# Optimization experiments

Measured on AMD Instinct MI355X. Metric: run time of the kernel, lower is better.

The kernel has to match this reference:

```python
import jax, jax.numpy as jnp
import numpy as np

EPS = 1e-06


def setup_inputs() -> dict:
    key = jax.random.key(0)
    k1, k2 = jax.random.split(key)
    x = jax.random.normal(k1, (256, 4096), dtype=jnp.float32)
    # learned parameter, init matches torch.randn(...) * 0.1
    shapelets = jax.random.normal(k2, (8, 16, 128), dtype=jnp.float32) * 0.1
    return {"x": x, "shapelets": shapelets}


def reference(x, shapelets):
    B, T = x.shape
    C, Kc, L = shapelets.shape
    nwin = T - L + 1  # stride-1 unfold

    # sliding windows: [B, nwin, L] (same materialization as torch unfold)
    idx = jnp.arange(nwin)[:, None] + jnp.arange(L)[None, :]
    x_win = x[:, idx]

    # z-normalize each window (population std, unbiased=False)
    mu_x = jnp.mean(x_win, axis=2, keepdims=True)
    var_x = jnp.mean((x_win - mu_x) ** 2, axis=2, keepdims=True)
    std_x = jnp.sqrt(var_x) + EPS
    x_norm = (x_win - mu_x) / std_x

    # z-normalize shapelets per class/shapelet
    mu_s = jnp.mean(shapelets, axis=2, keepdims=True)
    var_s = jnp.mean((shapelets - mu_s) ** 2, axis=2, keepdims=True)
    std_s = jnp.sqrt(var_s) + EPS
    s_norm = (shapelets - mu_s) / std_s

    # normalized cross-correlation: [B, nwin, C, Kc]
    corr = jnp.einsum('btl,ckl->btck', x_norm, s_norm) / L

    # max over window positions, concat classes -> [B, C*Kc]
    max_vals = jnp.max(corr, axis=1)  # [B, C, Kc]
    return max_vals.reshape(B, C * Kc)
```

## Files before the change

kernel.cpp:

```cpp
#include <hip/hip_runtime.h>
#include <hip/hip_bf16.h>

typedef __attribute__((ext_vector_type(8))) short short8;
typedef __attribute__((ext_vector_type(4))) float float4v;

#define T_LEN 4096
#define L_LEN 128
#define NWIN  3969
#define CK    128

__device__ __forceinline__ unsigned short f2bf(float f) {
    unsigned u = __float_as_uint(f);
    u += 0x7fffu + ((u >> 16) & 1u);
    return (unsigned short)(u >> 16);
}

__global__ void prep_sh(const float* __restrict__ sh,
                        unsigned short* __restrict__ wsB) {
    const int ck = blockIdx.x;
    const int l  = threadIdx.x;
    __shared__ float rs[2], rq[2];
    const int lane = l & 63, wv = l >> 6;

    float v = sh[ck * L_LEN + l];
    float s = v, q = v * v;
    #pragma unroll
    for (int off = 32; off >= 1; off >>= 1) {
        s += __shfl_xor(s, off);
        q += __shfl_xor(q, off);
    }
    if (lane == 0) { rs[wv] = s; rq[wv] = q; }
    __syncthreads();
    float sm = rs[0] + rs[1], sq = rq[0] + rq[1];
    float mu  = sm * (1.f / L_LEN);
    float var = fmaxf(sq * (1.f / L_LEN) - mu * mu, 0.f);
    float inv = 1.f / (sqrtf(var) + 1e-6f);
    unsigned short b = f2bf((v - mu) * inv);
    const int nt = ck >> 4, n = ck & 15;
    const int kt = l >> 5, qd = (l >> 3) & 3, jj = l & 7;
    wsB[((((nt * 4 + kt) * 64) + qd * 16 + n) << 3) + jj] = b;
}

__global__ __launch_bounds__(512, 2)
void conv_row(const float* __restrict__ x,
              const unsigned short* __restrict__ wsB,
              float* __restrict__ out) {
    __shared__ alignas(16) unsigned short xb[8][T_LEN];
    __shared__ float sty[T_LEN];
    __shared__ float PSs[513], PQs[513];
    __shared__ float grpS[8], grpQ[8];
    __shared__ float wmax[8][CK];

    const int tid  = threadIdx.x;
    const int lane = tid & 63;
    const int wv   = tid >> 6;
    const int row  = blockIdx.x;
    const float4* xr4 = (const float4*)(x + row * T_LEN);

    short8 Bf[8][4];
    {
        const short8* Bp = (const short8*)wsB;
        #pragma unroll
        for (int nt = 0; nt < 8; ++nt)
            #pragma unroll
            for (int kt = 0; kt < 4; ++kt)
                Bf[nt][kt] = Bp[(nt * 4 + kt) * 64 + lane];
    }

    float v[16];
    {
        float4 a0 = xr4[2 * tid];
        float4 a1 = xr4[2 * tid + 1];
        float4 a2 = make_float4(0.f, 0.f, 0.f, 0.f), a3 = a2;
        if (tid < 511) { a2 = xr4[2 * tid + 2]; a3 = xr4[2 * tid + 3]; }
        v[0]=a0.x; v[1]=a0.y; v[2]=a0.z;  v[3]=a0.w;
        v[4]=a1.x; v[5]=a1.y; v[6]=a1.z;  v[7]=a1.w;
        v[8]=a2.x; v[9]=a2.y; v[10]=a2.z; v[11]=a2.w;
        v[12]=a3.x; v[13]=a3.y; v[14]=a3.z; v[15]=a3.w;
    }
    unsigned short bb[16];
    #pragma unroll
    for (int i = 0; i < 16; ++i) bb[i] = f2bf(v[i]);
    #pragma unroll
    for (int c = 0; c < 8; ++c) {
        short8 w8;
        #pragma unroll
        for (int j = 0; j < 8; ++j) w8[j] = (short)bb[c + j];
        *(short8*)&xb[c][8 * tid] = w8;
    }

    float s = 0.f, q = 0.f;
    #pragma unroll
    for (int i = 0; i < 8; ++i) { s += v[i]; q += v[i] * v[i]; }
    float is = s, iq = q;
    #pragma unroll
    for (int off = 1; off < 64; off <<= 1) {
        float ts = __shfl_up(is, off);
        float tq = __shfl_up(iq, off);
        if (lane >= off) { is += ts; iq += tq; }
    }
    if (lane == 63) { grpS[wv] = is; grpQ[wv] = iq; }
    __syncthreads();
    float os = 0.f, oq = 0.f;
    #pragma unroll
    for (int w = 0; w < 7; ++w) if (w < wv) { os += grpS[w]; oq += grpQ[w]; }
    PSs[tid] = os + is - s;
    PQs[tid] = oq + iq - q;
    if (tid == 511) { PSs[512] = os + is; PQs[512] = oq + iq; }
    __syncthreads();

    if (tid < 497) {
        float S = PSs[tid + 16] - PSs[tid];
        float Q = PQs[tid + 16] - PQs[tid];
        float4 b0 = make_float4(0.f, 0.f, 0.f, 0.f), b1 = b0;
        if (tid <= 495) { b0 = xr4[2 * tid + 32]; b1 = xr4[2 * tid + 33]; }
        float xn[8] = {b0.x, b0.y, b0.z, b0.w, b1.x, b1.y, b1.z, b1.w};
        #pragma unroll
        for (int e = 0; e < 8; ++e) {
            int w = 8 * tid + e;
            if (w < NWIN) {
                float mu  = S * (1.f / L_LEN);
                float var = fmaxf(Q * (1.f / L_LEN) - mu * mu, 0.f);
                float sd  = sqrtf(var) + 1e-6f;
                sty[w] = 1.f / (sd * (float)L_LEN);
                S += xn[e] - v[e];
                Q += xn[e] * xn[e] - v[e] * v[e];
            }
        }
    }
    __syncthreads();

    const int abase = (lane & 15) + (lane >> 4);
    const int q4    = (lane >> 4) * 4;
    float vmax[8];
    #pragma unroll
    for (int nt = 0; nt < 8; ++nt) vmax[nt] = -1e30f;

    #pragma unroll 1
    for (int ii = 0; ii < 32; ++ii) {
        const int ci = (ii + 4 * wv) & 31;
        const int T0 = (ci < 31) ? ci * 128 : (NWIN - 128);
        const int e0 = T0 + wv;
        const int c  = e0 & 7;
        const int b8 = e0 >> 3;

        float sr[4];
        #pragma unroll
        for (int r = 0; r < 4; ++r) sr[r] = sty[e0 + 8 * (q4 + r)];
        short8 af[4];
        #pragma unroll
        for (int kt = 0; kt < 4; ++kt)
            af[kt] = *(const short8*)&xb[c][8 * (b8 + abase + 4 * kt)];

        float4v acc[8];
        #pragma unroll
        for (int nt = 0; nt < 8; ++nt) acc[nt] = float4v{0.f, 0.f, 0.f, 0.f};

        #pragma unroll
        for (int kt = 0; kt < 4; ++kt)
            #pragma unroll
            for (int nt = 0; nt < 8; ++nt)
                acc[nt] = __builtin_amdgcn_mfma_f32_16x16x32_bf16(
                    af[kt], Bf[nt][kt], acc[nt], 0, 0, 0);

        #pragma unroll
        for (int nt = 0; nt < 8; ++nt) {
            float m01 = fmaxf(acc[nt][0] * sr[0], acc[nt][1] * sr[1]);
            float m23 = fmaxf(acc[nt][2] * sr[2], acc[nt][3] * sr[3]);
            vmax[nt] = fmaxf(vmax[nt], fmaxf(m01, m23));
        }
    }

    #pragma unroll
    for (int nt = 0; nt < 8; ++nt) {
        float vx = vmax[nt];
        vx = fmaxf(vx, __shfl_xor(vx, 16));
        vx = fmaxf(vx, __shfl_xor(vx, 32));
        if (lane < 16) wmax[wv][nt * 16 + lane] = vx;
    }
    __syncthreads();
    if (tid < CK) {
        float m = wmax[0][tid];
        #pragma unroll
        for (int w = 1; w < 8; ++w) m = fmaxf(m, wmax[w][tid]);
        out[row * CK + tid] = m;
    }
}

extern "C" void kernel_launch(void* const* d_in, const int* in_sizes, int n_in,
                              void* d_out, int out_size, void* d_ws, size_t ws_size,
                              hipStream_t stream) {
    (void)in_sizes; (void)n_in; (void)out_size; (void)ws_size;
    const float* x  = (const float*)d_in[0];
    const float* sh = (const float*)d_in[1];
    unsigned short* wsB = (unsigned short*)d_ws;
    float* out = (float*)d_out;

    prep_sh<<<128, 128, 0, stream>>>(sh, wsB);
    conv_row<<<256, 512, 0, stream>>>(x, wsB, out);
}
```

Measured before the change: 82.21 us.

## Split shapelet columns across two wave halves with 1024-thread blocks

Doubles the block to 1024 threads and splits the 128 output columns between two groups of 8 waves. Each wave now holds half the B fragments and issues half the MFMAs per window tile. The first 512 threads still do the staging and stats, and the final max reduction is regrouped by column half. This is meant to raise wave-level parallelism per row, which matters because only 256 blocks cover the GPU. It costs idle threads during staging and tighter register limits from the 1024,4 launch bounds.

```diff
diff --git a/kernel.cpp b/kernel.cpp
--- a/kernel.cpp
+++ b/kernel.cpp
@@ -41,7 +41,7 @@
     wsB[((((nt * 4 + kt) * 64) + qd * 16 + n) << 3) + jj] = b;
 }
 
-__global__ __launch_bounds__(512, 2)
+__global__ __launch_bounds__(1024, 4)
 void conv_row(const float* __restrict__ x,
               const unsigned short* __restrict__ wsB,
               float* __restrict__ out) {
@@ -49,26 +49,29 @@
     __shared__ float sty[T_LEN];
     __shared__ float PSs[513], PQs[513];
     __shared__ float grpS[8], grpQ[8];
-    __shared__ float wmax[8][CK];
+    __shared__ float wmax[16][64];
 
     const int tid  = threadIdx.x;
     const int lane = tid & 63;
     const int wv   = tid >> 6;
     const int row  = blockIdx.x;
     const float4* xr4 = (const float4*)(x + row * T_LEN);
-
-    short8 Bf[8][4];
+    const bool stg = (tid < 512);
+
+    const int mg = wv & 7, nh = wv >> 3;
+    short8 Bf[4][4];
     {
         const short8* Bp = (const short8*)wsB;
         #pragma unroll
-        for (int nt = 0; nt < 8; ++nt)
+        for (int nt4 = 0; nt4 < 4; ++nt4)
             #pragma unroll
             for (int kt = 0; kt < 4; ++kt)
-                Bf[nt][kt] = Bp[(nt * 4 + kt) * 64 + lane];
+                Bf[nt4][kt] = Bp[((nh * 4 + nt4) * 4 + kt) * 64 + lane];
     }
 
     float v[16];
-    {
+    float s = 0.f, q = 0.f;
+    if (stg) {
         float4 a0 = xr4[2 * tid];
         float4 a1 = xr4[2 * tid + 1];
         float4 a2 = make_float4(0.f, 0.f, 0.f, 0.f), a3 = a2;
@@ -77,36 +80,43 @@
         v[4]=a1.x; v[5]=a1.y; v[6]=a1.z;  v[7]=a1.w;
         v[8]=a2.x; v[9]=a2.y; v[10]=a2.z; v[11]=a2.w;
         v[12]=a3.x; v[13]=a3.y; v[14]=a3.z; v[15]=a3.w;
-    }
-    unsigned short bb[16];
-    #pragma unroll
-    for (int i = 0; i < 16; ++i) bb[i] = f2bf(v[i]);
-    #pragma unroll
-    for (int c = 0; c < 8; ++c) {
-        short8 w8;
-        #pragma unroll
-        for (int j = 0; j < 8; ++j) w8[j] = (short)bb[c + j];
-        *(short8*)&xb[c][8 * tid] = w8;
-    }
-
-    float s = 0.f, q = 0.f;
-    #pragma unroll
-    for (int i = 0; i < 8; ++i) { s += v[i]; q += v[i] * v[i]; }
-    float is = s, iq = q;
-    #pragma unroll
-    for (int off = 1; off < 64; off <<= 1) {
-        float ts = __shfl_up(is, off);
-        float tq = __shfl_up(iq, off);
-        if (lane >= off) { is += ts; iq += tq; }
-    }
-    if (lane == 63) { grpS[wv] = is; grpQ[wv] = iq; }
-    __syncthreads();
-    float os = 0.f, oq = 0.f;
-    #pragma unroll
-    for (int w = 0; w < 7; ++w) if (w < wv) { os += grpS[w]; oq += grpQ[w]; }
-    PSs[tid] = os + is - s;
-    PQs[tid] = oq + iq - q;
-    if (tid == 511) { PSs[512] = os + is; PQs[512] = oq + iq; }
+
+        unsigned short bb[16];
+        #pragma unroll
+        for (int i = 0; i < 16; ++i) bb[i] = f2bf(v[i]);
+        #pragma unroll
+        for (int c = 0; c < 8; ++c) {
+            short8 w8;
+            #pragma unroll
+            for (int j = 0; j < 8; ++j) w8[j] = (short)bb[c + j];
+            *(short8*)&xb[c][8 * tid] = w8;
+        }
+
+        #pragma unroll
+        for (int i = 0; i < 8; ++i) { s += v[i]; q += v[i] * v[i]; }
+        float is = s, iq = q;
+        #pragma unroll
+        for (int off = 1; off < 64; off <<= 1) {
+            float ts = __shfl_up(is, off);
+            float tq = __shfl_up(iq, off);
+            if (lane >= off) { is += ts; iq += tq; }
+        }
+        if (lane == 63) { grpS[wv] = is; grpQ[wv] = iq; }
+        s = is; q = iq;
+    }
+    __syncthreads();
+    if (stg) {
+        float ss = s, qq = q;
+        float segs = 0.f, segq = 0.f;
+        #pragma unroll
+        for (int i = 0; i < 8; ++i) { segs += v[i]; segq += v[i] * v[i]; }
+        float os = 0.f, oq = 0.f;
+        #pragma unroll
+        for (int w = 0; w < 7; ++w) if (w < wv) { os += grpS[w]; oq += grpQ[w]; }
+        PSs[tid] = os + ss - segs;
+        PQs[tid] = oq + qq - segq;
+        if (tid == 511) { PSs[512] = os + ss; PQs[512] = oq + qq; }
+    }
     __syncthreads();
 
     if (tid < 497) {
@@ -132,15 +142,13 @@
 
     const int abase = (lane & 15) + (lane >> 4);
     const int q4    = (lane >> 4) * 4;
-    float vmax[8];
-    #pragma unroll
-    for (int nt = 0; nt < 8; ++nt) vmax[nt] = -1e30f;
+    float vmax[4] = {-1e30f, -1e30f, -1e30f, -1e30f};
 
     #pragma unroll 1
     for (int ii = 0; ii < 32; ++ii) {
-        const int ci = (ii + 4 * wv) & 31;
+        const int ci = (ii + 4 * mg) & 31;
         const int T0 = (ci < 31) ? ci * 128 : (NWIN - 128);
-        const int e0 = T0 + wv;
+        const int e0 = T0 + mg;
         const int c  = e0 & 7;
         const int b8 = e0 >> 3;
 
@@ -152,37 +160,38 @@
         for (int kt = 0; kt < 4; ++kt)
             af[kt] = *(const short8*)&xb[c][8 * (b8 + abase + 4 * kt)];
 
-        float4v acc[8];
-        #pragma unroll
-        for (int nt = 0; nt < 8; ++nt) acc[nt] = float4v{0.f, 0.f, 0.f, 0.f};
+        float4v acc[4];
+        #pragma unroll
+        for (int nt4 = 0; nt4 < 4; ++nt4) acc[nt4] = float4v{0.f, 0.f, 0.f, 0.f};
 
         #pragma unroll
         for (int kt = 0; kt < 4; ++kt)
             #pragma unroll
-            for (int nt = 0; nt < 8; ++nt)
-                acc[nt] = __builtin_amdgcn_mfma_f32_16x16x32_bf16(
-                    af[kt], Bf[nt][kt], acc[nt], 0, 0, 0);
-
-        #pragma unroll
-        for (int nt = 0; nt < 8; ++nt) {
-            float m01 = fmaxf(acc[nt][0] * sr[0], acc[nt][1] * sr[1]);
-            float m23 = fmaxf(acc[nt][2] * sr[2], acc[nt][3] * sr[3]);
-            vmax[nt] = fmaxf(vmax[nt], fmaxf(m01, m23));
+            for (int nt4 = 0; nt4 < 4; ++nt4)
+                acc[nt4] = __builtin_amdgcn_mfma_f32_16x16x32_bf16(
+                    af[kt], Bf[nt4][kt], acc[nt4], 0, 0, 0);
+
+        #pragma unroll
+        for (int nt4 = 0; nt4 < 4; ++nt4) {
+            float m01 = fmaxf(acc[nt4][0] * sr[0], acc[nt4][1] * sr[1]);
+            float m23 = fmaxf(acc[nt4][2] * sr[2], acc[nt4][3] * sr[3]);
+            vmax[nt4] = fmaxf(vmax[nt4], fmaxf(m01, m23));
         }
     }
 
     #pragma unroll
-    for (int nt = 0; nt < 8; ++nt) {
-        float vx = vmax[nt];
+    for (int nt4 = 0; nt4 < 4; ++nt4) {
+        float vx = vmax[nt4];
         vx = fmaxf(vx, __shfl_xor(vx, 16));
         vx = fmaxf(vx, __shfl_xor(vx, 32));
-        if (lane < 16) wmax[wv][nt * 16 + lane] = vx;
+        if (lane < 16) wmax[wv][nt4 * 16 + lane] = vx;
     }
     __syncthreads();
     if (tid < CK) {
-        float m = wmax[0][tid];
-        #pragma unroll
-        for (int w = 1; w < 8; ++w) m = fmaxf(m, wmax[w][tid]);
+        const int h = tid >> 6, idx = tid & 63;
+        float m = wmax[8 * h][idx];
+        #pragma unroll
+        for (int g = 1; g < 8; ++g) m = fmaxf(m, wmax[8 * h + g][idx]);
         out[row * CK + tid] = m;
     }
 }
@@ -197,5 +206,5 @@
     float* out = (float*)d_out;
 
     prep_sh<<<128, 128, 0, stream>>>(sh, wsB);
-    conv_row<<<256, 512, 0, stream>>>(x, wsB, out);
-}
+    conv_row<<<256, 1024, 0, stream>>>(x, wsB, out);
+}
```

Result: no change. 83.54 us (+1.6%).

## Software-pipeline MFMA tiles with double-buffered fragments and accumulators

Applied to the files above, without the earlier changes.

Restructures the per-wave chunk loop into a two-stage software pipeline. LDS loads for the next tile and the max-reduction epilogue of the previous tile are interleaved with the current tile's MFMA burst. The first MFMA takes a zero accumulator so no separate zero-init is needed. This aims to hide LDS latency and epilogue ALU work behind matrix ops, at the cost of doubling accumulator and fragment registers, which risks spills under the existing launch bounds.

```diff
diff --git a/kernel.cpp b/kernel.cpp
--- a/kernel.cpp
+++ b/kernel.cpp
@@ -132,44 +132,72 @@
 
     const int abase = (lane & 15) + (lane >> 4);
     const int q4    = (lane >> 4) * 4;
+    const float4v z4 = float4v{0.f, 0.f, 0.f, 0.f};
+
     float vmax[8];
     #pragma unroll
     for (int nt = 0; nt < 8; ++nt) vmax[nt] = -1e30f;
 
-    #pragma unroll 1
-    for (int ii = 0; ii < 32; ++ii) {
-        const int ci = (ii + 4 * wv) & 31;
-        const int T0 = (ci < 31) ? ci * 128 : (NWIN - 128);
-        const int e0 = T0 + wv;
-        const int c  = e0 & 7;
-        const int b8 = e0 >> 3;
-
-        float sr[4];
+    short8  afA[4], afB[4];
+    float4v accA[8], accB[8];
+    float4v srA, srB;
+
+    auto T0of = [&](int c) {
+        int ci = (c + 4 * wv) & 31;
+        return (ci < 31) ? ci * 128 : (NWIN - 128);
+    };
+    auto loadA = [&](int c, short8 af[4]) {
+        const int e0 = T0of(c) + wv;
+        const int cc = e0 & 7, b8 = e0 >> 3;
+        #pragma unroll
+        for (int kt = 0; kt < 4; ++kt)
+            af[kt] = *(const short8*)&xb[cc][8 * (b8 + abase + 4 * kt)];
+    };
+    auto loadS = [&](int c, float4v& sr) {
+        const int e0 = T0of(c) + wv;
         #pragma unroll
         for (int r = 0; r < 4; ++r) sr[r] = sty[e0 + 8 * (q4 + r)];
-        short8 af[4];
-        #pragma unroll
-        for (int kt = 0; kt < 4; ++kt)
-            af[kt] = *(const short8*)&xb[c][8 * (b8 + abase + 4 * kt)];
-
-        float4v acc[8];
-        #pragma unroll
-        for (int nt = 0; nt < 8; ++nt) acc[nt] = float4v{0.f, 0.f, 0.f, 0.f};
-
-        #pragma unroll
-        for (int kt = 0; kt < 4; ++kt)
+    };
+    auto burst = [&](const short8 af[4], float4v acc[8]) {
+        #pragma unroll
+        for (int nt = 0; nt < 8; ++nt)
+            acc[nt] = __builtin_amdgcn_mfma_f32_16x16x32_bf16(
+                af[0], Bf[nt][0], z4, 0, 0, 0);
+        #pragma unroll
+        for (int kt = 1; kt < 4; ++kt)
             #pragma unroll
             for (int nt = 0; nt < 8; ++nt)
                 acc[nt] = __builtin_amdgcn_mfma_f32_16x16x32_bf16(
                     af[kt], Bf[nt][kt], acc[nt], 0, 0, 0);
-
+    };
+    auto epi = [&](const float4v acc[8], const float4v& sr) {
         #pragma unroll
         for (int nt = 0; nt < 8; ++nt) {
-            float m01 = fmaxf(acc[nt][0] * sr[0], acc[nt][1] * sr[1]);
-            float m23 = fmaxf(acc[nt][2] * sr[2], acc[nt][3] * sr[3]);
-            vmax[nt] = fmaxf(vmax[nt], fmaxf(m01, m23));
+            float4v t = acc[nt] * sr;
+            vmax[nt] = fmaxf(vmax[nt],
+                             fmaxf(fmaxf(t[0], t[1]), fmaxf(t[2], t[3])));
         }
-    }
+    };
+
+    loadA(0, afA); loadS(0, srA);
+    burst(afA, accA);
+    loadA(1, afB); loadS(1, srB);
+    burst(afB, accB);
+    loadA(2, afA);
+    epi(accA, srA);
+
+    #pragma unroll 1
+    for (int p = 1; p <= 15; ++p) {
+        loadS(2 * p, srA);
+        burst(afA, accA);
+        loadA(2 * p + 1, afB);
+        epi(accB, srB);
+        loadS(2 * p + 1, srB);
+        burst(afB, accB);
+        loadA(2 * p + 2, afA);
+        epi(accA, srA);
+    }
+    epi(accB, srB);
 
     #pragma unroll
     for (int nt = 0; nt < 8; ++nt) {
```

After: 84.00 us. 2.2% more time.
